# Performance work log

Measured on AMD Instinct MI355X. Metric: run time of the kernel, lower is better.

The kernel has to match this reference:

```python
import jax, jax.numpy as jnp
import numpy as np

N_NODES = 2000
N_EDGES = 40000
DILATION = 2
DC = 32  # dilation_channels
C_IN = 32  # in_channels (= gcn out_channels)


def setup_inputs() -> dict:
    key = jax.random.key(0)
    ks = jax.random.split(key, 8)
    x = jax.random.normal(ks[0], (4, 34, N_NODES, C_IN), jnp.float32)
    edge_index = jax.random.randint(ks[1], (2, N_EDGES), 0, N_NODES, dtype=jnp.int64)
    edge_weight = jax.random.uniform(ks[2], (N_EDGES,), jnp.float32)
    gate1_w = jax.random.normal(ks[3], (DC, C_IN, 1, 2), jnp.float32) * 0.1
    gate1_b = jnp.zeros((DC,), jnp.float32)
    gate2_w = jax.random.normal(ks[4], (DC, C_IN, 1, 2), jnp.float32) * 0.1
    gate2_b = jnp.zeros((DC,), jnp.float32)
    gcn_w = jax.random.normal(ks[5], (DC, C_IN), jnp.float32) * 0.1
    gcn_b = jnp.zeros((C_IN,), jnp.float32)
    return {"x": x, "edge_index": edge_index, "edge_weight": edge_weight,
            "gate1_w": gate1_w, "gate1_b": gate1_b,
            "gate2_w": gate2_w, "gate2_b": gate2_b,
            "gcn_w": gcn_w, "gcn_b": gcn_b}


def _gate_conv(x_nchw, w, b):
    # Conv2d(kernel=(1,2), dilation=DILATION), VALID padding -> acts on time (W) axis
    y = jax.lax.conv_general_dilated(
        x_nchw, w, window_strides=(1, 1), padding='VALID',
        rhs_dilation=(1, DILATION),
        dimension_numbers=('NCHW', 'OIHW', 'NCHW'))
    return y + b[None, :, None, None]


def reference(x, edge_index, edge_weight, gate1_w, gate1_b, gate2_w, gate2_b, gcn_w, gcn_b):
    B, T, N, C = x.shape
    xt = jnp.transpose(x, (0, 3, 2, 1))  # (B, C, N, T)
    g1 = jnp.tanh(_gate_conv(xt, gate1_w, gate1_b))      # (B, DC, N, T')
    g2 = jax.nn.sigmoid(_gate_conv(xt, gate2_w, gate2_b))
    g = g1 * g2
    Tp = g.shape[-1]
    h = jnp.transpose(g, (0, 3, 2, 1)).reshape(B * Tp, N, DC)  # (Bt, N, DC)

    # GCN normalization with self loops (PyG gcn_norm, add_self_loops=True)
    row, col = edge_index[0], edge_index[1]
    loop = jnp.arange(N, dtype=edge_index.dtype)
    row_f = jnp.concatenate([row, loop])
    col_f = jnp.concatenate([col, loop])
    w_f = jnp.concatenate([edge_weight, jnp.ones((N,), edge_weight.dtype)])
    deg = jax.ops.segment_sum(w_f, col_f, num_segments=N)
    dis = jnp.where(deg > 0, jax.lax.rsqrt(deg), 0.0)
    norm = dis[row_f] * w_f * dis[col_f]  # (E+N,)

    hw = jnp.einsum('bnd,de->bne', h, gcn_w)          # (Bt, N, C_IN)
    msgs = hw[:, row_f, :] * norm[None, :, None]      # (Bt, E+N, C_IN)
    out = jnp.zeros_like(hw).at[:, col_f, :].add(msgs) + gcn_b  # scatter over targets

    return out.reshape(B, Tp, N, C_IN)  # (B, T', N, in_channels)
```

## Files before the change

kernel.cpp:

```cpp
#include <hip/hip_runtime.h>
#include <hip/hip_bf16.h>

typedef short short8 __attribute__((ext_vector_type(8)));
typedef float floatx4 __attribute__((ext_vector_type(4)));
typedef float float2v __attribute__((ext_vector_type(2)));
typedef unsigned uint4v __attribute__((ext_vector_type(4)));

#define NN 2000
#define NE 40000
#define NB 4
#define T_IN 34
#define TP 32
#define NBT (NB * TP)
#define CAP 96
#define NEB 157


__device__ inline unsigned short f2bf(float x) {
    unsigned int u = __float_as_uint(x);
    u = u + 0x7fff + ((u >> 16) & 1);
    return (unsigned short)(u >> 16);
}
__device__ inline void splitPair(float x0, float x1, unsigned& hi, unsigned& lo) {
    unsigned u0 = __float_as_uint(x0), u1 = __float_as_uint(x1);
    hi = __builtin_amdgcn_perm(u1, u0, 0x07060302u);
    float r0 = x0 - __uint_as_float(u0 & 0xffff0000u);
    float r1 = x1 - __uint_as_float(u1 & 0xffff0000u);
    lo = __builtin_amdgcn_perm(__float_as_uint(r1), __float_as_uint(r0), 0x07060302u);
}
__device__ inline void splitA8(const float* v, short8& hi, short8& lo) {
    union { unsigned u[4]; short8 s; } H, L;
#pragma unroll
    for (int j = 0; j < 4; ++j) {
        unsigned h_, l_;
        splitPair(v[2 * j], v[2 * j + 1], h_, l_);
        H.u[j] = h_; L.u[j] = l_;
    }
    hi = H.s; lo = L.s;
}

__global__ __launch_bounds__(256) void conv_deg_kernel(
        const float* __restrict__ x,
        const float* __restrict__ w1, const float* __restrict__ b1,
        const float* __restrict__ w2, const float* __restrict__ b2,
        unsigned* __restrict__ h2,
        const int* __restrict__ row, const int* __restrict__ col,
        const float* __restrict__ ew,
        float* __restrict__ deg, int* __restrict__ cursor,
        int2* __restrict__ pcsr) {
    if (blockIdx.x < NEB) {
        int e = blockIdx.x * 256 + threadIdx.x;
        if (e < NE) {
            int c = col[e], r = row[e];
            float w = ew[e];
            atomicAdd(&deg[c], w);
            int slot = atomicAdd(&cursor[c], 1);
            if (slot < CAP) pcsr[c * CAP + slot] = make_int2(r, __float_as_int(w));
        }
        return;
    }

    int l = threadIdx.x & 63;
    int w = threadIdx.x >> 6;
    int colL = l & 15, q = l >> 4;

    short8 Whi[2][2][2], Wlo[2][2][2];
#pragma unroll
    for (int g = 0; g < 2; ++g) {
        const float* wp = g ? w2 : w1;
#pragma unroll
        for (int d = 0; d < 2; ++d)
#pragma unroll
        for (int tap = 0; tap < 2; ++tap) {
            float wv[8];
#pragma unroll
            for (int j = 0; j < 8; ++j)
                wv[j] = wp[(d * 16 + colL) * 64 + (q * 8 + j) * 2 + tap];
            splitA8(wv, Whi[g][d][tap], Wlo[g][d][tap]);
        }
    }
    float bias[2][2] = { { b1[colL], b1[colL + 16] }, { b2[colL], b2[colL + 16] } };

    int cb = blockIdx.x - NEB;
    int ntile = cb % 125;
    int b_ = cb / 125;
    int tb = w;
    int n0 = ntile * 16;
    int t0 = tb * 8;

    const float* xw = x + (((size_t)b_ * T_IN * NN) + n0 + colL) * 32 + q * 8;
    auto LD = [&](int t, float* vdst) {
        const float* p = xw + (size_t)t * (NN * 32);
        *(float4*)vdst       = *(const float4*)p;
        *(float4*)(vdst + 4) = *(const float4*)(p + 4);
    };

    float v[3][8];
    short8 shi[3], slo[3];
    LD(t0, v[0]); LD(t0 + 1, v[1]); LD(t0 + 2, v[2]);
    splitA8(v[0], shi[0], slo[0]);
    splitA8(v[1], shi[1], slo[1]);

#pragma unroll
    for (int j = 0; j < 8; ++j) {
        const int c0 = j % 3;
        const int c2 = (j + 2) % 3;
        splitA8(v[c2], shi[c2], slo[c2]);
        if (j < 7) LD(t0 + j + 3, v[c0]);

        floatx4 acc[2][2];
#pragma unroll
        for (int g = 0; g < 2; ++g)
#pragma unroll
        for (int d = 0; d < 2; ++d) {
            float bv = bias[g][d];
            floatx4 a = { bv, bv, bv, bv };
            a = __builtin_amdgcn_mfma_f32_16x16x32_bf16(shi[c0], Whi[g][d][0], a, 0, 0, 0);
            a = __builtin_amdgcn_mfma_f32_16x16x32_bf16(shi[c2], Whi[g][d][1], a, 0, 0, 0);
            a = __builtin_amdgcn_mfma_f32_16x16x32_bf16(slo[c0], Whi[g][d][0], a, 0, 0, 0);
            a = __builtin_amdgcn_mfma_f32_16x16x32_bf16(slo[c2], Whi[g][d][1], a, 0, 0, 0);
            a = __builtin_amdgcn_mfma_f32_16x16x32_bf16(shi[c0], Wlo[g][d][0], a, 0, 0, 0);
            a = __builtin_amdgcn_mfma_f32_16x16x32_bf16(shi[c2], Wlo[g][d][1], a, 0, 0, 0);
            acc[g][d] = a;
        }

        int bt = b_ * TP + t0 + j;
#pragma unroll
        for (int r = 0; r < 4; ++r) {
            float g10 = acc[0][0][r], g20 = acc[1][0][r];
            float g11 = acc[0][1][r], g21 = acc[1][1][r];
            float e20 = __expf(2.0f * g10);
            float th0 = (e20 - 1.0f) / (e20 + 1.0f);
            float sg0 = 1.0f / (1.0f + __expf(-g20));
            float e21 = __expf(2.0f * g11);
            float th1 = (e21 - 1.0f) / (e21 + 1.0f);
            float sg1 = 1.0f / (1.0f + __expf(-g21));
            unsigned pk = (unsigned)f2bf(th0 * sg0) | ((unsigned)f2bf(th1 * sg1) << 16);
            int n = n0 + q * 4 + r;
            h2[(n * NBT + bt) * 16 + colL] = pk;
        }
    }
}

__device__ inline void acc8(float2v* a2, uint4v u, float2v nr2) {
#pragma unroll
    for (int j = 0; j < 4; ++j) {
        float2v vv;
        vv.x = __uint_as_float(u[j] << 16);
        vv.y = __uint_as_float(u[j] & 0xffff0000u);
        asm("v_pk_fma_f32 %0, %1, %2, %0" : "+v"(a2[j]) : "v"(vv), "v"(nr2));
    }
}

__global__ __launch_bounds__(256) void agg_gcn_kernel(
        const unsigned* __restrict__ h2,
        const float* __restrict__ deg, const int* __restrict__ cursor,
        const int2* __restrict__ pcsr,
        const float* __restrict__ gw, const float* __restrict__ gb,
        float* __restrict__ out) {
    __shared__ float st[64 * 36];
    int l = threadIdx.x & 63;
    int wv = threadIdx.x >> 6;
    int b = blockIdx.x;
    int cp = b & 7;
    int n = (b >> 3) * 4 + wv;
    int colL = l & 15, q = l >> 4;

    short8 Bhi[2], Blo[2];
#pragma unroll
    for (int d = 0; d < 2; ++d) {
        float wv8[8];
#pragma unroll
        for (int j = 0; j < 8; ++j)
            wv8[j] = gw[(q * 8 + j) * 32 + d * 16 + colL];
        splitA8(wv8, Bhi[d], Blo[d]);
    }
    float gb0 = gb[colL], gb1 = gb[colL + 16];

    const unsigned* base = h2 + cp * 256 + l * 4;
    float dn = rsqrtf(deg[n] + 1.0f);
    float2v a2[4] = { {0,0}, {0,0}, {0,0}, {0,0} };
    {
        float w0 = dn * dn;
        uint4v sv = *(const uint4v*)(base + (size_t)n * 2048);
        acc8(a2, sv, (float2v){ w0, w0 });
    }
    int cnt = cursor[n]; if (cnt > CAP) cnt = CAP;
    const int2* slots = pcsr + n * CAP;
    int i = 0;
    for (; i + 8 <= cnt; i += 8) {
        int2 e0 = slots[i],     e1 = slots[i + 1], e2 = slots[i + 2], e3 = slots[i + 3];
        int2 e4 = slots[i + 4], e5 = slots[i + 5], e6 = slots[i + 6], e7 = slots[i + 7];
        float n0 = rsqrtf(deg[e0.x] + 1.0f) * __int_as_float(e0.y) * dn;
        float n1 = rsqrtf(deg[e1.x] + 1.0f) * __int_as_float(e1.y) * dn;
        float n2 = rsqrtf(deg[e2.x] + 1.0f) * __int_as_float(e2.y) * dn;
        float n3 = rsqrtf(deg[e3.x] + 1.0f) * __int_as_float(e3.y) * dn;
        float n4 = rsqrtf(deg[e4.x] + 1.0f) * __int_as_float(e4.y) * dn;
        float n5 = rsqrtf(deg[e5.x] + 1.0f) * __int_as_float(e5.y) * dn;
        float n6 = rsqrtf(deg[e6.x] + 1.0f) * __int_as_float(e6.y) * dn;
        float n7 = rsqrtf(deg[e7.x] + 1.0f) * __int_as_float(e7.y) * dn;
        uint4v v0 = *(const uint4v*)(base + (size_t)e0.x * 2048);
        uint4v v1 = *(const uint4v*)(base + (size_t)e1.x * 2048);
        uint4v v2 = *(const uint4v*)(base + (size_t)e2.x * 2048);
        uint4v v3 = *(const uint4v*)(base + (size_t)e3.x * 2048);
        uint4v v4 = *(const uint4v*)(base + (size_t)e4.x * 2048);
        uint4v v5 = *(const uint4v*)(base + (size_t)e5.x * 2048);
        uint4v v6 = *(const uint4v*)(base + (size_t)e6.x * 2048);
        uint4v v7 = *(const uint4v*)(base + (size_t)e7.x * 2048);
        acc8(a2, v0, (float2v){n0, n0}); acc8(a2, v1, (float2v){n1, n1});
        acc8(a2, v2, (float2v){n2, n2}); acc8(a2, v3, (float2v){n3, n3});
        acc8(a2, v4, (float2v){n4, n4}); acc8(a2, v5, (float2v){n5, n5});
        acc8(a2, v6, (float2v){n6, n6}); acc8(a2, v7, (float2v){n7, n7});
    }
    for (; i + 4 <= cnt; i += 4) {
        int2 e0 = slots[i], e1 = slots[i + 1], e2 = slots[i + 2], e3 = slots[i + 3];
        float n0 = rsqrtf(deg[e0.x] + 1.0f) * __int_as_float(e0.y) * dn;
        float n1 = rsqrtf(deg[e1.x] + 1.0f) * __int_as_float(e1.y) * dn;
        float n2 = rsqrtf(deg[e2.x] + 1.0f) * __int_as_float(e2.y) * dn;
        float n3 = rsqrtf(deg[e3.x] + 1.0f) * __int_as_float(e3.y) * dn;
        uint4v v0 = *(const uint4v*)(base + (size_t)e0.x * 2048);
        uint4v v1 = *(const uint4v*)(base + (size_t)e1.x * 2048);
        uint4v v2 = *(const uint4v*)(base + (size_t)e2.x * 2048);
        uint4v v3 = *(const uint4v*)(base + (size_t)e3.x * 2048);
        acc8(a2, v0, (float2v){n0, n0}); acc8(a2, v1, (float2v){n1, n1});
        acc8(a2, v2, (float2v){n2, n2}); acc8(a2, v3, (float2v){n3, n3});
    }
    for (; i < cnt; ++i) {
        int2 e0 = slots[i];
        float n0 = rsqrtf(deg[e0.x] + 1.0f) * __int_as_float(e0.y) * dn;
        uint4v v0 = *(const uint4v*)(base + (size_t)e0.x * 2048);
        acc8(a2, v0, (float2v){n0, n0});
    }

    float* dst = &st[(wv * 16 + (l >> 2)) * 36 + (l & 3) * 4];
    *(float4*)dst        = make_float4(a2[0].x, a2[1].x, a2[2].x, a2[3].x);
    *(float4*)(dst + 16) = make_float4(a2[0].y, a2[1].y, a2[2].y, a2[3].y);
    __syncthreads();

    float av[8];
    const float* ap = &st[(wv * 16 + colL) * 36 + q * 8];
    *(float4*)av       = *(const float4*)ap;
    *(float4*)(av + 4) = *(const float4*)(ap + 4);
    short8 Ahi, Alo;
    splitA8(av, Ahi, Alo);
    floatx4 z = { 0.f, 0.f, 0.f, 0.f };
    floatx4 acc0 = z, acc1 = z;
    acc0 = __builtin_amdgcn_mfma_f32_16x16x32_bf16(Ahi, Bhi[0], acc0, 0, 0, 0);
    acc0 = __builtin_amdgcn_mfma_f32_16x16x32_bf16(Alo, Bhi[0], acc0, 0, 0, 0);
    acc0 = __builtin_amdgcn_mfma_f32_16x16x32_bf16(Ahi, Blo[0], acc0, 0, 0, 0);
    acc1 = __builtin_amdgcn_mfma_f32_16x16x32_bf16(Ahi, Bhi[1], acc1, 0, 0, 0);
    acc1 = __builtin_amdgcn_mfma_f32_16x16x32_bf16(Alo, Bhi[1], acc1, 0, 0, 0);
    acc1 = __builtin_amdgcn_mfma_f32_16x16x32_bf16(Ahi, Blo[1], acc1, 0, 0, 0);
#pragma unroll
    for (int r = 0; r < 4; ++r) {
        int btl = q * 4 + r;
        size_t o = ((size_t)(cp * 16 + btl) * NN + n) << 5;
        out[o + colL]      = acc0[r] + gb0;
        out[o + colL + 16] = acc1[r] + gb1;
    }
}

extern "C" void kernel_launch(void* const* d_in, const int* in_sizes, int n_in,
                              void* d_out, int out_size, void* d_ws, size_t ws_size,
                              hipStream_t stream) {
    const float* x   = (const float*)d_in[0];
    const int*   ei  = (const int*)d_in[1];
    const float* ew  = (const float*)d_in[2];
    const float* g1w = (const float*)d_in[3];
    const float* g1b = (const float*)d_in[4];
    const float* g2w = (const float*)d_in[5];
    const float* g2b = (const float*)d_in[6];
    const float* gcw = (const float*)d_in[7];
    const float* gcb = (const float*)d_in[8];
    float* out = (float*)d_out;

    float* wsf      = (float*)d_ws;
    float* deg      = wsf;
    int*   cursor   = (int*)(wsf + 2048);
    int2*  pcsr     = (int2*)(wsf + 4096);
    unsigned* h2    = (unsigned*)(wsf + 388096);

    const int* row = ei;
    const int* col = ei + NE;

    hipMemsetAsync(wsf, 0, 4096 * sizeof(float), stream);
    hipLaunchKernelGGL(conv_deg_kernel, dim3(NEB + 500), dim3(256), 0, stream,
                       x, g1w, g1b, g2w, g2b, h2, row, col, ew,
                       deg, cursor, pcsr);
    hipLaunchKernelGGL(agg_gcn_kernel, dim3(4000), dim3(256), 0, stream,
                       h2, deg, cursor, pcsr, gcw, gcb, out);
}
```

Measured before the change: 150.7 us.

## Remap conv tiles to flat position order and front-load all input loads

The gated conv part now gives each wave four 16-node tiles indexed over a flattened (bt, node) space, with each tile holding one output time step. All input loads (both dilation taps) are issued up front, before the weight setup. This replaces the per-wave sliding 8-timestep window with its 3-slot rolling buffer, and the conv grid doubles. Each x row is now loaded twice (once per tap) instead of being reused across timesteps. The intent is more memory-level parallelism and more blocks to hide latency, at the cost of redundant reads.

New measurement: 153.8 us. +2.1%, slower.

```diff
diff --git a/kernel.cpp b/kernel.cpp
--- a/kernel.cpp
+++ b/kernel.cpp
@@ -63,6 +63,25 @@
     int l = threadIdx.x & 63;
     int w = threadIdx.x >> 6;
     int colL = l & 15, q = l >> 4;
+    int cb = blockIdx.x - NEB;
+
+    float va[4][8], vb[4][8];
+    int n0s[4], bts[4];
+#pragma unroll
+    for (int i = 0; i < 4; ++i) {
+        int tile = cb * 16 + w * 4 + i;
+        int pos0 = tile * 16;
+        int bt = pos0 / 2000;
+        int n0 = pos0 - bt * 2000;
+        n0s[i] = n0; bts[i] = bt;
+        int b_ = bt >> 5, t_ = bt & 31;
+        const float* xa = x + (((b_ * T_IN + t_) * NN) + n0 + colL) * 32 + q * 8;
+        const float* xb = xa + 2 * NN * 32;
+        *(float4*)&va[i][0] = *(const float4*)xa;
+        *(float4*)&va[i][4] = *(const float4*)(xa + 4);
+        *(float4*)&vb[i][0] = *(const float4*)xb;
+        *(float4*)&vb[i][4] = *(const float4*)(xb + 4);
+    }
 
     short8 Whi[2][2][2], Wlo[2][2][2];
 #pragma unroll
@@ -81,32 +100,11 @@
     }
     float bias[2][2] = { { b1[colL], b1[colL + 16] }, { b2[colL], b2[colL + 16] } };
 
-    int cb = blockIdx.x - NEB;
-    int ntile = cb % 125;
-    int b_ = cb / 125;
-    int tb = w;
-    int n0 = ntile * 16;
-    int t0 = tb * 8;
-
-    const float* xw = x + (((size_t)b_ * T_IN * NN) + n0 + colL) * 32 + q * 8;
-    auto LD = [&](int t, float* vdst) {
-        const float* p = xw + (size_t)t * (NN * 32);
-        *(float4*)vdst       = *(const float4*)p;
-        *(float4*)(vdst + 4) = *(const float4*)(p + 4);
-    };
-
-    float v[3][8];
-    short8 shi[3], slo[3];
-    LD(t0, v[0]); LD(t0 + 1, v[1]); LD(t0 + 2, v[2]);
-    splitA8(v[0], shi[0], slo[0]);
-    splitA8(v[1], shi[1], slo[1]);
-
-#pragma unroll
-    for (int j = 0; j < 8; ++j) {
-        const int c0 = j % 3;
-        const int c2 = (j + 2) % 3;
-        splitA8(v[c2], shi[c2], slo[c2]);
-        if (j < 7) LD(t0 + j + 3, v[c0]);
+#pragma unroll
+    for (int i = 0; i < 4; ++i) {
+        short8 Ahi0, Alo0, Ahi1, Alo1;
+        splitA8(va[i], Ahi0, Alo0);
+        splitA8(vb[i], Ahi1, Alo1);
 
         floatx4 acc[2][2];
 #pragma unroll
@@ -115,16 +113,16 @@
         for (int d = 0; d < 2; ++d) {
             float bv = bias[g][d];
             floatx4 a = { bv, bv, bv, bv };
-            a = __builtin_amdgcn_mfma_f32_16x16x32_bf16(shi[c0], Whi[g][d][0], a, 0, 0, 0);
-            a = __builtin_amdgcn_mfma_f32_16x16x32_bf16(shi[c2], Whi[g][d][1], a, 0, 0, 0);
-            a = __builtin_amdgcn_mfma_f32_16x16x32_bf16(slo[c0], Whi[g][d][0], a, 0, 0, 0);
-            a = __builtin_amdgcn_mfma_f32_16x16x32_bf16(slo[c2], Whi[g][d][1], a, 0, 0, 0);
-            a = __builtin_amdgcn_mfma_f32_16x16x32_bf16(shi[c0], Wlo[g][d][0], a, 0, 0, 0);
-            a = __builtin_amdgcn_mfma_f32_16x16x32_bf16(shi[c2], Wlo[g][d][1], a, 0, 0, 0);
+            a = __builtin_amdgcn_mfma_f32_16x16x32_bf16(Ahi0, Whi[g][d][0], a, 0, 0, 0);
+            a = __builtin_amdgcn_mfma_f32_16x16x32_bf16(Ahi1, Whi[g][d][1], a, 0, 0, 0);
+            a = __builtin_amdgcn_mfma_f32_16x16x32_bf16(Alo0, Whi[g][d][0], a, 0, 0, 0);
+            a = __builtin_amdgcn_mfma_f32_16x16x32_bf16(Alo1, Whi[g][d][1], a, 0, 0, 0);
+            a = __builtin_amdgcn_mfma_f32_16x16x32_bf16(Ahi0, Wlo[g][d][0], a, 0, 0, 0);
+            a = __builtin_amdgcn_mfma_f32_16x16x32_bf16(Ahi1, Wlo[g][d][1], a, 0, 0, 0);
             acc[g][d] = a;
         }
 
-        int bt = b_ * TP + t0 + j;
+        int n0 = n0s[i], bt = bts[i];
 #pragma unroll
         for (int r = 0; r < 4; ++r) {
             float g10 = acc[0][0][r], g20 = acc[1][0][r];
@@ -284,7 +282,7 @@
     const int* col = ei + NE;
 
     hipMemsetAsync(wsf, 0, 4096 * sizeof(float), stream);
-    hipLaunchKernelGGL(conv_deg_kernel, dim3(NEB + 500), dim3(256), 0, stream,
+    hipLaunchKernelGGL(conv_deg_kernel, dim3(NEB + 1000), dim3(256), 0, stream,
                        x, g1w, g1b, g2w, g2b, h2, row, col, ew,
                        deg, cursor, pcsr);
     hipLaunchKernelGGL(agg_gcn_kernel, dim3(4000), dim3(256), 0, stream,
```
